# Performance work log

Hardware: AMD Instinct MI355X
Metric: run time of the kernel (lower is better)

## Reference

```python
import jax, jax.numpy as jnp
import numpy as np
import math

B, T, D = 8, 1024, 1024
N, L = 256, 768
H = 16
TE = 2048  # time_embed_dim
EPS = 1e-5


def _ln(x, g, b):
    mu = jnp.mean(x, axis=-1, keepdims=True)
    var = jnp.mean(jnp.square(x - mu), axis=-1, keepdims=True)
    return (x - mu) * jax.lax.rsqrt(var + EPS) * g + b


def setup_inputs() -> dict:
    key = jax.random.key(0)
    ks = jax.random.split(key, 16)
    s = lambda fan_in: 1.0 / math.sqrt(fan_in)
    return {
        "x": jax.random.normal(ks[0], (B, T, D), jnp.float32),
        "xf": jax.random.normal(ks[1], (B, N, L), jnp.float32),
        "emb": jax.random.normal(ks[2], (B, TE), jnp.float32),
        "ln_g": jnp.ones((D,), jnp.float32),
        "ln_b": jnp.zeros((D,), jnp.float32),
        "cln_g": jnp.ones((L,), jnp.float32),
        "cln_b": jnp.zeros((L,), jnp.float32),
        "Wq": jax.random.normal(ks[3], (D, D), jnp.float32) * s(D),
        "bq": jnp.zeros((D,), jnp.float32),
        "Wk": jax.random.normal(ks[4], (L, D), jnp.float32) * s(L),
        "bk": jnp.zeros((D,), jnp.float32),
        "Wv": jax.random.normal(ks[5], (L, D), jnp.float32) * s(L),
        "bv": jnp.zeros((D,), jnp.float32),
        "sln_g": jnp.ones((D,), jnp.float32),
        "sln_b": jnp.zeros((D,), jnp.float32),
        "Wemb": jax.random.normal(ks[6], (TE, 2 * D), jnp.float32) * s(TE),
        "bemb": jnp.zeros((2 * D,), jnp.float32),
        "Wout": jax.random.normal(ks[7], (D, D), jnp.float32) * s(D) * 0.02,
        "bout": jnp.zeros((D,), jnp.float32),
    }


def reference(x, xf, emb, ln_g, ln_b, cln_g, cln_b, Wq, bq, Wk, bk, Wv, bv,
              sln_g, sln_b, Wemb, bemb, Wout, bout):
    # x: (B,T,D), xf: (B,N,L), emb: (B,TE)
    hd = D // H
    q = (_ln(x, ln_g, ln_b) @ Wq + bq).reshape(B, T, H, hd)
    xf_n = _ln(xf, cln_g, cln_b)
    k = (xf_n @ Wk + bk).reshape(B, N, H, hd)
    v = (xf_n @ Wv + bv).reshape(B, N, H, hd)
    # scores: (B,T,N,H); note: scaled by sqrt(D//H)
    att = jnp.einsum('bthd,bnhd->btnh', q, k) / math.sqrt(hd)
    w = jax.nn.softmax(att, axis=2)  # softmax over conditioning tokens N
    y = jnp.einsum('btnh,bnhd->bthd', w, v).reshape(B, T, D)
    # StylizationBlock (dropout = 0)
    emb_out = jax.nn.silu(emb) @ Wemb + bemb  # (B, 2D)
    scale, shift = jnp.split(emb_out[:, None, :], 2, axis=2)
    h = _ln(y, sln_g, sln_b) * (1.0 + scale) + shift
    h = jax.nn.silu(h) @ Wout + bout
    return x + h
```

## Files before the change

kernel.cpp:

```cpp
#include <hip/hip_runtime.h>
#include <hip/hip_bf16.h>

typedef __hip_bfloat16 bf16;
typedef unsigned short ushort;
typedef unsigned char uchar;
typedef long i64;
typedef __attribute__((ext_vector_type(8))) short bf16x8;
typedef __attribute__((ext_vector_type(4))) float f32x4;

#define B_ 8
#define T_ 1024
#define D_ 1024
#define N_ 256
#define L_ 768
#define H_ 16
#define HD_ 64
#define TE_ 2048

__device__ __forceinline__ void gld16(const void* g, void* l) {
    __builtin_amdgcn_global_load_lds((const __attribute__((address_space(1))) void*)g,
                                     (__attribute__((address_space(3))) void*)l,
                                     16, 0, 0);
}

__device__ __forceinline__ float bitf(unsigned u) { return __uint_as_float(u); }

__device__ __forceinline__ int pk4_fp8(float a, float b, float c, float d) {
    int p = __builtin_amdgcn_cvt_pk_fp8_f32(a, b, 0, false);
    p = __builtin_amdgcn_cvt_pk_fp8_f32(c, d, p, true);
    return p;
}
__device__ __forceinline__ uchar pk1_fp8(float a) {
    int p = __builtin_amdgcn_cvt_pk_fp8_f32(a, a, 0, false);
    return (uchar)(p & 0xff);
}

__global__ __launch_bounds__(256) void prep_kernel(
        const float* __restrict__ x, const float* __restrict__ xf,
        const float* __restrict__ g1, const float* __restrict__ b1,
        const float* __restrict__ g2, const float* __restrict__ b2,
        const float* __restrict__ Wq, const float* __restrict__ Wk,
        const float* __restrict__ Wv, const float* __restrict__ Wo,
        const float* __restrict__ emb, const float* __restrict__ Wemb,
        uchar* __restrict__ xn8, uchar* __restrict__ xfn8,
        uchar* __restrict__ wq8, uchar* __restrict__ wk8,
        uchar* __restrict__ wv8, uchar* __restrict__ wo8,
        float* __restrict__ part) {
    __shared__ __align__(16) char smem[16384];
    int bid = blockIdx.x;
    int tid = threadIdx.x;
    if (bid < 10240) {
        const float *rp, *g, *bb; uchar* op; int cols;
        if (bid < B_ * T_) {
            rp = x + (size_t)bid * D_; g = g1; bb = b1; op = xn8 + (size_t)bid * D_; cols = D_;
        } else {
            int r = bid - B_ * T_;
            rp = xf + (size_t)r * L_; g = g2; bb = b2; op = xfn8 + (size_t)r * L_; cols = L_;
        }
        float* ps  = (float*)smem;
        float* ps2 = ps + 4;
        float* st  = ps + 8;
        bool act = tid * 4 < cols;
        float4 v = act ? *(const float4*)&rp[tid * 4] : make_float4(0.f, 0.f, 0.f, 0.f);
        float s = v.x + v.y + v.z + v.w;
        float s2 = v.x * v.x + v.y * v.y + v.z * v.z + v.w * v.w;
        for (int off = 32; off; off >>= 1) {
            s  += __shfl_down(s,  off, 64);
            s2 += __shfl_down(s2, off, 64);
        }
        int wid = tid >> 6, lid = tid & 63;
        if (lid == 0) { ps[wid] = s; ps2[wid] = s2; }
        __syncthreads();
        if (tid == 0) {
            float t = ps[0] + ps[1] + ps[2] + ps[3];
            float t2 = ps2[0] + ps2[1] + ps2[2] + ps2[3];
            float m = t / cols;
            float var = t2 / cols - m * m;
            st[0] = m; st[1] = rsqrtf(var + 1e-5f);
        }
        __syncthreads();
        if (!act) return;
        float mu = st[0], rstd = st[1];
        float4 gv = *(const float4*)&g[tid * 4];
        float4 bv = *(const float4*)&bb[tid * 4];
        float o0 = (v.x - mu) * rstd * gv.x + bv.x;
        float o1 = (v.y - mu) * rstd * gv.y + bv.y;
        float o2 = (v.z - mu) * rstd * gv.z + bv.z;
        float o3 = (v.w - mu) * rstd * gv.w + bv.w;
        *(int*)&op[tid * 4] = pk4_fp8(o0, o1, o2, o3);
    } else if (bid < 11136) {
        uchar (*t)[65] = (uchar(*)[65])smem;
        int id = bid - 10240;
        int xb = id & 15, y = id >> 4;
        const float* W; uchar* Wt; int K, ky;
        if (y < 16)      { W = Wq; Wt = wq8; K = 1024; ky = y; }
        else if (y < 28) { W = Wk; Wt = wk8; K = 768;  ky = y - 16; }
        else if (y < 40) { W = Wv; Wt = wv8; K = 768;  ky = y - 28; }
        else             { W = Wo; Wt = wo8; K = 1024; ky = y - 40; }
        int k0 = ky * 64, n0 = xb * 64;
#pragma unroll
        for (int i = 0; i < 16; i++) {
            int e = tid + i * 256;
            int r = e >> 6, c = e & 63;
            t[r][c] = pk1_fp8(W[(size_t)(k0 + r) * D_ + n0 + c]);
        }
        __syncthreads();
#pragma unroll
        for (int i = 0; i < 4; i++) {
            int e = tid + i * 256;
            int r = e >> 4, cg = (e & 15) * 4;
            unsigned u = (unsigned)t[cg][r] | ((unsigned)t[cg + 1][r] << 8)
                       | ((unsigned)t[cg + 2][r] << 16) | ((unsigned)t[cg + 3][r] << 24);
            *(unsigned*)&Wt[(size_t)(n0 + r) * K + k0 + cg] = u;
        }
    } else {
        float* se  = (float*)smem;
        float* red = (float*)(smem + 8192);
        int id = bid - 11136;
        int j0 = (id & 31) * 64;
        int ks = id >> 5;
        int tx = tid & 15, ty = tid >> 4;
        int w = tid >> 6, lane = tid & 63;
#pragma unroll
        for (int b = 0; b < 8; b++) {
            float xv = emb[b * TE_ + ks * 256 + tid];
            se[b * 256 + tid] = xv / (1.f + __expf(-xv));
        }
        __syncthreads();
        float acc[8][4] = {};
#pragma unroll 4
        for (int i = 0; i < 16; i++) {
            int e = ty + 16 * i;
            float4 wv = *(const float4*)&Wemb[(size_t)(ks * 256 + e) * 2048 + j0 + tx * 4];
#pragma unroll
            for (int b = 0; b < 8; b++) {
                float s = se[b * 256 + e];
                acc[b][0] += s * wv.x; acc[b][1] += s * wv.y;
                acc[b][2] += s * wv.z; acc[b][3] += s * wv.w;
            }
        }
#pragma unroll
        for (int b = 0; b < 8; b++)
#pragma unroll
            for (int m = 0; m < 4; m++) {
                float v = acc[b][m];
                v += __shfl_down(v, 32, 64);
                v += __shfl_down(v, 16, 64);
                if (lane < 16) red[(w * 8 + b) * 64 + lane * 4 + m] = v;
            }
        __syncthreads();
        for (int o = tid; o < 512; o += 256) {
            int b = o >> 6, jl = o & 63;
            float s = red[(0 * 8 + b) * 64 + jl] + red[(1 * 8 + b) * 64 + jl]
                    + red[(2 * 8 + b) * 64 + jl] + red[(3 * 8 + b) * 64 + jl];
            part[((size_t)ks * 8 + b) * 2048 + j0 + jl] = s;
        }
    }
}

template <int MODE>
__device__ __forceinline__ void gemm_body(const uchar* __restrict__ Ap,
                                          const uchar* __restrict__ Bp,
                                          const float* __restrict__ bias,
                                          const float* __restrict__ res,
                                          void* __restrict__ Cout,
                                          int m0, int n0, int Ncols, int K,
                                          uchar* Ash, uchar* Bsh) {
    int tid = threadIdx.x;
    int w = tid >> 6, lane = tid & 63;
    int quad = lane >> 4, l15 = lane & 15;
    int wm = (w >> 1) * 64, wn = (w & 1) * 32;
    int lr8 = lane >> 3;
    int sc  = lane & 7;
    int gc  = sc ^ lr8;
    f32x4 acc[4][2] = {};
    for (int kt = 0; kt < K; kt += 128) {
#pragma unroll
        for (int j = 0; j < 4; j++) {
            int rbase = w * 32 + j * 8;
            gld16(&Ap[(size_t)(m0 + rbase + lr8) * K + kt + gc * 16], &Ash[rbase * 128]);
        }
#pragma unroll
        for (int j = 0; j < 2; j++) {
            int rbase = w * 16 + j * 8;
            gld16(&Bp[(size_t)(n0 + rbase + lr8) * K + kt + gc * 16], &Bsh[rbase * 128]);
        }
        __syncthreads();
#pragma unroll
        for (int kh = 0; kh < 4; kh++) {
            int c4 = kh * 2 + (quad >> 1);
            int sub = (quad & 1) * 8;
            int pos = (c4 ^ (l15 & 7)) * 16 + sub;
            i64 af[4], bfr[2];
#pragma unroll
            for (int mt = 0; mt < 4; mt++)
                af[mt] = *(const i64*)&Ash[(wm + mt * 16 + l15) * 128 + pos];
#pragma unroll
            for (int nt = 0; nt < 2; nt++)
                bfr[nt] = *(const i64*)&Bsh[(wn + nt * 16 + l15) * 128 + pos];
#pragma unroll
            for (int mt = 0; mt < 4; mt++)
#pragma unroll
                for (int nt = 0; nt < 2; nt++)
                    acc[mt][nt] = __builtin_amdgcn_mfma_f32_16x16x32_fp8_fp8(af[mt], bfr[nt], acc[mt][nt], 0, 0, 0);
        }
        __syncthreads();
    }
#pragma unroll
    for (int mt = 0; mt < 4; mt++) {
#pragma unroll
        for (int nt = 0; nt < 2; nt++) {
#pragma unroll
            for (int reg = 0; reg < 4; reg++) {
                int row = m0 + wm + mt * 16 + quad * 4 + reg;
                int col = n0 + wn + nt * 16 + l15;
                float v = acc[mt][nt][reg] + bias[col];
                if (MODE == 1) {
                    v += res[(size_t)row * Ncols + col];
                    ((float*)Cout)[(size_t)row * Ncols + col] = v;
                } else if (MODE == 0) {
                    ((bf16*)Cout)[(size_t)row * Ncols + col] = __float2bfloat16(v);
                } else {
                    int b = row >> 8, n = row & 255;
                    int h = col >> 6, d = col & 63;
                    size_t addr = ((size_t)(b * 16 + h) * 64 + d) * 256
                                + (((n >> 3) ^ (d & 7)) * 8) + (n & 7);
                    ((bf16*)Cout)[addr] = __float2bfloat16(v);
                }
            }
        }
    }
}

__global__ __launch_bounds__(256) void qkv_gemm(const uchar* __restrict__ xn8,
                                                const uchar* __restrict__ xfn8,
                                                const uchar* __restrict__ wq8,
                                                const uchar* __restrict__ wk8,
                                                const uchar* __restrict__ wv8,
                                                const float* __restrict__ bq,
                                                const float* __restrict__ bk,
                                                const float* __restrict__ bv,
                                                bf16* __restrict__ q,
                                                bf16* __restrict__ kbuf,
                                                bf16* __restrict__ vT,
                                                const float* __restrict__ part,
                                                const float* __restrict__ bemb,
                                                float* __restrict__ embo) {
    __shared__ __align__(16) uchar Ash[128 * 128];
    __shared__ __align__(16) uchar Bsh[64 * 128];
    int bid = blockIdx.x;
    if (bid < 1024) {
        gemm_body<0>(xn8, wq8, bq, nullptr, q,
                     (bid & 63) * 128, (bid >> 6) * 64, D_, D_, Ash, Bsh);
    } else if (bid < 1280) {
        int id = bid - 1024;
        gemm_body<0>(xfn8, wk8, bk, nullptr, kbuf,
                     (id & 15) * 128, (id >> 4) * 64, D_, L_, Ash, Bsh);
    } else if (bid < 1536) {
        int id = bid - 1280;
        gemm_body<2>(xfn8, wv8, bv, nullptr, vT,
                     (id & 15) * 128, (id >> 4) * 64, D_, L_, Ash, Bsh);
    } else {
        int o = (bid - 1536) * 256 + threadIdx.x;
        int b = o >> 11, j = o & 2047;
        float s = bemb[j];
#pragma unroll
        for (int ks = 0; ks < 8; ks++) s += part[((size_t)ks * 8 + b) * 2048 + j];
        embo[o] = s;
    }
}

__global__ __launch_bounds__(256) void out_gemm(const uchar* __restrict__ a8,
                                                const uchar* __restrict__ wo8,
                                                const float* __restrict__ bout,
                                                const float* __restrict__ x,
                                                float* __restrict__ out) {
    __shared__ __align__(16) uchar Ash[128 * 128];
    __shared__ __align__(16) uchar Bsh[64 * 128];
    int bid = blockIdx.x;
    gemm_body<1>(a8, wo8, bout, x, out,
                 (bid & 63) * 128, (bid >> 6) * 64, D_, D_, Ash, Bsh);
}

__global__ __launch_bounds__(256) void attn_mfma(const bf16* __restrict__ q,
                                                 const bf16* __restrict__ k,
                                                 const bf16* __restrict__ vT,
                                                 bf16* __restrict__ y) {
    __shared__ ushort KV[N_ * HD_];
    __shared__ ushort P[64 * N_];
    int tid = threadIdx.x;
    int w = tid >> 6, lane = tid & 63;
    int quad = lane >> 4, l15 = lane & 15;
    int t0 = blockIdx.x * 64;
    int bh = blockIdx.y;
    int b = bh >> 4, h = bh & 15;

    const ushort* kp = (const ushort*)k;
    const ushort* qp = (const ushort*)q;
    const ushort* vp = (const ushort*)vT;
    int lr8 = lane >> 3, sc = lane & 7, gc = sc ^ lr8;

#pragma unroll
    for (int j = 0; j < 8; j++) {
        int rbase = w * 64 + j * 8;
        gld16(&kp[(size_t)(b * N_ + rbase + lr8) * D_ + h * 64 + gc * 8], &KV[rbase * 64]);
    }
#pragma unroll
    for (int j = 0; j < 2; j++) {
        int rbase = w * 16 + j * 8;
        gld16(&qp[(size_t)(b * T_ + t0 + rbase + lr8) * D_ + h * 64 + gc * 8], &P[rbase * 64]);
    }
    __syncthreads();

    int qrow = w * 16 + l15;
    bf16x8 aq[2];
#pragma unroll
    for (int kk = 0; kk < 2; kk++)
        aq[kk] = *(bf16x8*)&P[qrow * 64 + (((kk * 4 + quad) ^ (qrow & 7)) * 8)];
    f32x4 sf[16];
#pragma unroll
    for (int nt = 0; nt < 16; nt++) {
        int n = nt * 16 + l15;
        bf16x8 b0 = *(bf16x8*)&KV[n * 64 + (((0 + quad) ^ (n & 7)) * 8)];
        bf16x8 b1 = *(bf16x8*)&KV[n * 64 + (((4 + quad) ^ (n & 7)) * 8)];
        f32x4 z = {};
        f32x4 t = __builtin_amdgcn_mfma_f32_16x16x32_bf16(aq[0], b0, z, 0, 0, 0);
        sf[nt] = __builtin_amdgcn_mfma_f32_16x16x32_bf16(aq[1], b1, t, 0, 0, 0);
    }
    __syncthreads();

    const ushort* vbase = vp + (size_t)(b * 16 + h) * 16384;
#pragma unroll
    for (int j = 0; j < 8; j++) {
        gld16(&vbase[(w * 8 + j) * 512 + lane * 8], &KV[(w * 8 + j) * 512]);
    }

    const float scale = 0.125f;
    float mx[4] = {-1e30f, -1e30f, -1e30f, -1e30f};
#pragma unroll
    for (int nt = 0; nt < 16; nt++)
#pragma unroll
        for (int reg = 0; reg < 4; reg++) mx[reg] = fmaxf(mx[reg], sf[nt][reg]);
#pragma unroll
    for (int off = 1; off < 16; off <<= 1)
#pragma unroll
        for (int reg = 0; reg < 4; reg++)
            mx[reg] = fmaxf(mx[reg], __shfl_xor(mx[reg], off, 64));
    float sm[4] = {0.f, 0.f, 0.f, 0.f};
#pragma unroll
    for (int nt = 0; nt < 16; nt++)
#pragma unroll
        for (int reg = 0; reg < 4; reg++) {
            float e = __expf((sf[nt][reg] - mx[reg]) * scale);
            sf[nt][reg] = e;
            sm[reg] += e;
        }
#pragma unroll
    for (int off = 1; off < 16; off <<= 1)
#pragma unroll
        for (int reg = 0; reg < 4; reg++)
            sm[reg] += __shfl_xor(sm[reg], off, 64);
    float inv[4];
#pragma unroll
    for (int reg = 0; reg < 4; reg++) inv[reg] = 1.f / sm[reg];

#pragma unroll
    for (int nt = 0; nt < 16; nt++)
#pragma unroll
        for (int reg = 0; reg < 4; reg++) {
            int r = w * 16 + quad * 4 + reg;
            int colc = nt * 2 + (l15 >> 3);
            int addr = r * 256 + ((colc ^ (r & 7)) * 8) + (l15 & 7);
            bf16 hv = __float2bfloat16(sf[nt][reg]);
            P[addr] = *(ushort*)&hv;
        }
    __syncthreads();

    f32x4 of[4] = {};
    int prow = w * 16 + l15;
#pragma unroll
    for (int kk = 0; kk < 8; kk++) {
        bf16x8 ap = *(bf16x8*)&P[prow * 256 + (((kk * 4 + quad) ^ (prow & 7)) * 8)];
#pragma unroll
        for (int dt = 0; dt < 4; dt++) {
            int d = dt * 16 + l15;
            bf16x8 bv = *(bf16x8*)&KV[d * 256 + (((kk * 4 + quad) ^ (d & 7)) * 8)];
            of[dt] = __builtin_amdgcn_mfma_f32_16x16x32_bf16(ap, bv, of[dt], 0, 0, 0);
        }
    }
#pragma unroll
    for (int dt = 0; dt < 4; dt++)
#pragma unroll
        for (int reg = 0; reg < 4; reg++) {
            int r = t0 + w * 16 + quad * 4 + reg;
            y[((size_t)(b * T_ + r) * D_) + h * 64 + dt * 16 + l15] =
                __float2bfloat16(of[dt][reg] * inv[reg]);
        }
}

__global__ __launch_bounds__(256) void styl_kernel(const bf16* __restrict__ y,
                                                   const float* __restrict__ g,
                                                   const float* __restrict__ bb,
                                                   const float* __restrict__ embo,
                                                   uchar* __restrict__ a8) {
    int row = blockIdx.x;
    int b = row >> 10;
    int tid = threadIdx.x;
    const ushort* rp = (const ushort*)(y + (size_t)row * D_);
    ushort4 uy = *(const ushort4*)&rp[tid * 4];
    float v0 = bitf((unsigned)uy.x << 16), v1 = bitf((unsigned)uy.y << 16);
    float v2 = bitf((unsigned)uy.z << 16), v3 = bitf((unsigned)uy.w << 16);
    float s = v0 + v1 + v2 + v3;
    float s2 = v0 * v0 + v1 * v1 + v2 * v2 + v3 * v3;
    for (int off = 32; off; off >>= 1) {
        s  += __shfl_down(s,  off, 64);
        s2 += __shfl_down(s2, off, 64);
    }
    __shared__ float ps[4], ps2[4];
    __shared__ float smu, srstd;
    int wid = tid >> 6, lid = tid & 63;
    if (lid == 0) { ps[wid] = s; ps2[wid] = s2; }
    __syncthreads();
    if (tid == 0) {
        float t = ps[0] + ps[1] + ps[2] + ps[3];
        float t2 = ps2[0] + ps2[1] + ps2[2] + ps2[3];
        float m = t / D_;
        float var = t2 / D_ - m * m;
        smu = m; srstd = rsqrtf(var + 1e-5f);
    }
    __syncthreads();
    float mu = smu, rstd = srstd;
    float4 gv = *(const float4*)&g[tid * 4];
    float4 bv = *(const float4*)&bb[tid * 4];
    float4 scv = *(const float4*)&embo[b * 2048 + tid * 4];
    float4 shv = *(const float4*)&embo[b * 2048 + 1024 + tid * 4];
    float n0 = (v0 - mu) * rstd * gv.x + bv.x;
    float n1 = (v1 - mu) * rstd * gv.y + bv.y;
    float n2 = (v2 - mu) * rstd * gv.z + bv.z;
    float n3 = (v3 - mu) * rstd * gv.w + bv.w;
    float h0 = n0 * (1.f + scv.x) + shv.x;
    float h1 = n1 * (1.f + scv.y) + shv.y;
    float h2 = n2 * (1.f + scv.z) + shv.z;
    float h3 = n3 * (1.f + scv.w) + shv.w;
    h0 = h0 / (1.f + __expf(-h0));
    h1 = h1 / (1.f + __expf(-h1));
    h2 = h2 / (1.f + __expf(-h2));
    h3 = h3 / (1.f + __expf(-h3));
    *(int*)&a8[(size_t)row * D_ + tid * 4] = pk4_fp8(h0, h1, h2, h3);
}

extern "C" void kernel_launch(void* const* d_in, const int* in_sizes, int n_in,
                              void* d_out, int out_size, void* d_ws, size_t ws_size,
                              hipStream_t stream) {
    const float* x    = (const float*)d_in[0];
    const float* xf   = (const float*)d_in[1];
    const float* emb  = (const float*)d_in[2];
    const float* ln_g = (const float*)d_in[3];
    const float* ln_b = (const float*)d_in[4];
    const float* cln_g= (const float*)d_in[5];
    const float* cln_b= (const float*)d_in[6];
    const float* Wq   = (const float*)d_in[7];
    const float* bq   = (const float*)d_in[8];
    const float* Wk   = (const float*)d_in[9];
    const float* bk   = (const float*)d_in[10];
    const float* Wv   = (const float*)d_in[11];
    const float* bv   = (const float*)d_in[12];
    const float* sln_g= (const float*)d_in[13];
    const float* sln_b= (const float*)d_in[14];
    const float* Wemb = (const float*)d_in[15];
    const float* bemb = (const float*)d_in[16];
    const float* Wout = (const float*)d_in[17];
    const float* bout = (const float*)d_in[18];
    float* out = (float*)d_out;

    char* wsp = (char*)d_ws;
    const size_t MB = 1024 * 1024;
    uchar* xn8  = (uchar*)(wsp);
    uchar* xfn8 = (uchar*)(wsp + 8 * MB);
    uchar* wq8  = (uchar*)(wsp + 10 * MB);
    uchar* wk8  = (uchar*)(wsp + 11 * MB);
    uchar* wv8  = (uchar*)(wsp + 12 * MB);
    uchar* wo8  = (uchar*)(wsp + 13 * MB);
    bf16*  q    = (bf16*)(wsp + 14 * MB);
    bf16*  kbuf = (bf16*)(wsp + 30 * MB);
    bf16*  vT   = (bf16*)(wsp + 34 * MB);
    bf16*  ybuf = (bf16*)(wsp + 38 * MB);
    uchar* a8   = (uchar*)(wsp + 54 * MB);
    float* embo = (float*)(wsp + 62 * MB);
    float* part = (float*)(wsp + 63 * MB);

    prep_kernel<<<11392, 256, 0, stream>>>(x, xf, ln_g, ln_b, cln_g, cln_b,
                                           Wq, Wk, Wv, Wout, emb, Wemb,
                                           xn8, xfn8, wq8, wk8, wv8, wo8, part);

    qkv_gemm<<<1600, 256, 0, stream>>>(xn8, xfn8, wq8, wk8, wv8, bq, bk, bv,
                                       q, kbuf, vT, part, bemb, embo);

    attn_mfma<<<dim3(16, 128), 256, 0, stream>>>(q, kbuf, vT, ybuf);

    styl_kernel<<<B_ * T_, 256, 0, stream>>>(ybuf, sln_g, sln_b, embo, a8);

    out_gemm<<<1024, 256, 0, stream>>>(a8, wo8, bout, x, out);
}
```

Baseline: 242.0 us.

## Double-buffer LDS tiles in the fp8 GEMM body to overlap loads with MFMA

The GEMM main loop now ping-pongs between two LDS buffers for A and B. The next K-tile's global-to-LDS loads are issued before the MFMA work on the current tile, and one barrier per iteration replaces two. The goal is to hide global load latency behind matrix math in the QKV and output GEMMs. The cost is double the shared memory per block (about 48KB), which can lower the number of resident blocks per CU.

```diff
diff --git a/kernel.cpp b/kernel.cpp
--- a/kernel.cpp
+++ b/kernel.cpp
@@ -165,7 +165,8 @@
                                           const float* __restrict__ res,
                                           void* __restrict__ Cout,
                                           int m0, int n0, int Ncols, int K,
-                                          uchar* Ash, uchar* Bsh) {
+                                          uchar* Ash0, uchar* Ash1,
+                                          uchar* Bsh0, uchar* Bsh1) {
     int tid = threadIdx.x;
     int w = tid >> 6, lane = tid & 63;
     int quad = lane >> 4, l15 = lane & 15;
@@ -174,18 +175,36 @@
     int sc  = lane & 7;
     int gc  = sc ^ lr8;
     f32x4 acc[4][2] = {};
-    for (int kt = 0; kt < K; kt += 128) {
-#pragma unroll
-        for (int j = 0; j < 4; j++) {
-            int rbase = w * 32 + j * 8;
-            gld16(&Ap[(size_t)(m0 + rbase + lr8) * K + kt + gc * 16], &Ash[rbase * 128]);
-        }
-#pragma unroll
-        for (int j = 0; j < 2; j++) {
-            int rbase = w * 16 + j * 8;
-            gld16(&Bp[(size_t)(n0 + rbase + lr8) * K + kt + gc * 16], &Bsh[rbase * 128]);
-        }
+#pragma unroll
+    for (int j = 0; j < 4; j++) {
+        int rbase = w * 32 + j * 8;
+        gld16(&Ap[(size_t)(m0 + rbase + lr8) * K + gc * 16], &Ash0[rbase * 128]);
+    }
+#pragma unroll
+    for (int j = 0; j < 2; j++) {
+        int rbase = w * 16 + j * 8;
+        gld16(&Bp[(size_t)(n0 + rbase + lr8) * K + gc * 16], &Bsh0[rbase * 128]);
+    }
+    int nk = K >> 7;
+    for (int ki = 0; ki < nk; ki++) {
         __syncthreads();
+        uchar* Acur = (ki & 1) ? Ash1 : Ash0;
+        uchar* Bcur = (ki & 1) ? Bsh1 : Bsh0;
+        if (ki + 1 < nk) {
+            uchar* Anxt = (ki & 1) ? Ash0 : Ash1;
+            uchar* Bnxt = (ki & 1) ? Bsh0 : Bsh1;
+            int kt = (ki + 1) << 7;
+#pragma unroll
+            for (int j = 0; j < 4; j++) {
+                int rbase = w * 32 + j * 8;
+                gld16(&Ap[(size_t)(m0 + rbase + lr8) * K + kt + gc * 16], &Anxt[rbase * 128]);
+            }
+#pragma unroll
+            for (int j = 0; j < 2; j++) {
+                int rbase = w * 16 + j * 8;
+                gld16(&Bp[(size_t)(n0 + rbase + lr8) * K + kt + gc * 16], &Bnxt[rbase * 128]);
+            }
+        }
 #pragma unroll
         for (int kh = 0; kh < 4; kh++) {
             int c4 = kh * 2 + (quad >> 1);
@@ -194,17 +213,16 @@
             i64 af[4], bfr[2];
 #pragma unroll
             for (int mt = 0; mt < 4; mt++)
-                af[mt] = *(const i64*)&Ash[(wm + mt * 16 + l15) * 128 + pos];
+                af[mt] = *(const i64*)&Acur[(wm + mt * 16 + l15) * 128 + pos];
 #pragma unroll
             for (int nt = 0; nt < 2; nt++)
-                bfr[nt] = *(const i64*)&Bsh[(wn + nt * 16 + l15) * 128 + pos];
+                bfr[nt] = *(const i64*)&Bcur[(wn + nt * 16 + l15) * 128 + pos];
 #pragma unroll
             for (int mt = 0; mt < 4; mt++)
 #pragma unroll
                 for (int nt = 0; nt < 2; nt++)
                     acc[mt][nt] = __builtin_amdgcn_mfma_f32_16x16x32_fp8_fp8(af[mt], bfr[nt], acc[mt][nt], 0, 0, 0);
         }
-        __syncthreads();
     }
 #pragma unroll
     for (int mt = 0; mt < 4; mt++) {
@@ -246,20 +264,23 @@
                                                 const float* __restrict__ part,
                                                 const float* __restrict__ bemb,
                                                 float* __restrict__ embo) {
-    __shared__ __align__(16) uchar Ash[128 * 128];
-    __shared__ __align__(16) uchar Bsh[64 * 128];
+    __shared__ __align__(16) uchar Ash[2][128 * 128];
+    __shared__ __align__(16) uchar Bsh[2][64 * 128];
     int bid = blockIdx.x;
     if (bid < 1024) {
         gemm_body<0>(xn8, wq8, bq, nullptr, q,
-                     (bid & 63) * 128, (bid >> 6) * 64, D_, D_, Ash, Bsh);
+                     (bid & 63) * 128, (bid >> 6) * 64, D_, D_,
+                     Ash[0], Ash[1], Bsh[0], Bsh[1]);
     } else if (bid < 1280) {
         int id = bid - 1024;
         gemm_body<0>(xfn8, wk8, bk, nullptr, kbuf,
-                     (id & 15) * 128, (id >> 4) * 64, D_, L_, Ash, Bsh);
+                     (id & 15) * 128, (id >> 4) * 64, D_, L_,
+                     Ash[0], Ash[1], Bsh[0], Bsh[1]);
     } else if (bid < 1536) {
         int id = bid - 1280;
         gemm_body<2>(xfn8, wv8, bv, nullptr, vT,
-                     (id & 15) * 128, (id >> 4) * 64, D_, L_, Ash, Bsh);
+                     (id & 15) * 128, (id >> 4) * 64, D_, L_,
+                     Ash[0], Ash[1], Bsh[0], Bsh[1]);
     } else {
         int o = (bid - 1536) * 256 + threadIdx.x;
         int b = o >> 11, j = o & 2047;
@@ -275,11 +296,12 @@
                                                 const float* __restrict__ bout,
                                                 const float* __restrict__ x,
                                                 float* __restrict__ out) {
-    __shared__ __align__(16) uchar Ash[128 * 128];
-    __shared__ __align__(16) uchar Bsh[64 * 128];
+    __shared__ __align__(16) uchar Ash[2][128 * 128];
+    __shared__ __align__(16) uchar Bsh[2][64 * 128];
     int bid = blockIdx.x;
     gemm_body<1>(a8, wo8, bout, x, out,
-                 (bid & 63) * 128, (bid >> 6) * 64, D_, D_, Ash, Bsh);
+                 (bid & 63) * 128, (bid >> 6) * 64, D_, D_,
+                 Ash[0], Ash[1], Bsh[0], Bsh[1]);
 }
 
 __global__ __launch_bounds__(256) void attn_mfma(const bf16* __restrict__ q,
```

Result: no change. 246.5 us (+1.8%).
